# Performance work log

Measured on AMD Instinct MI355X. Metric: run time of the kernel, lower is better.

The kernel has to match this reference:

```python
import jax, jax.numpy as jnp
import numpy as np

B, W, N, K = 8, 16, 40, 10
DN = DL = 128
DE = 128
H = 4
NEG_SLOPE = 0.2


def _build_graph():
    # per-graph ring adjacency: i -> (i+d) % N for d=1..K, in dense_to_sparse order (src-major, dst ascending)
    src0, dst0 = [], []
    for i in range(N):
        ds = sorted(((i + d) % N) for d in range(1, K + 1))
        src0 += [i] * K
        dst0 += ds
    src0 = np.asarray(src0)
    dst0 = np.asarray(dst0)
    G = B * W
    Epg = N * K
    offs = np.arange(G)[:, None] * N
    node_adj = np.stack([(src0[None] + offs).reshape(-1), (dst0[None] + offs).reshape(-1)])
    # line graph: for each node, pair every incoming edge with every outgoing edge (torch repeat/tile order)
    a0, a1, fe = [], [], []
    for num in range(N):
        inc = np.nonzero(dst0 == num)[0]
        out = np.nonzero(src0 == num)[0]
        a0.append(np.repeat(inc, out.size))
        a1.append(np.tile(out, inc.size))
        fe.append(np.full(inc.size * out.size, num))
    a0, a1, fe = np.concatenate(a0), np.concatenate(a1), np.concatenate(fe)
    keep = a0 != a1  # remove_self_loops (no-op here, kept for fidelity)
    a0, a1, fe = a0[keep], a1[keep], fe[keep]
    eoffs = np.arange(G)[:, None] * Epg
    edge_adj = np.stack([(a0[None] + eoffs).reshape(-1), (a1[None] + eoffs).reshape(-1)])
    edge_efea = (fe[None] + offs).reshape(-1)
    return node_adj, edge_adj, edge_efea


def setup_inputs() -> dict:
    key = jax.random.key(0)
    node_adj, edge_adj, edge_efea = _build_graph()
    Epg = N * K
    D1 = DN + DL
    ks = jax.random.split(key, 16)

    def lin(k, fi, fo):
        return jax.random.normal(k, (fi, fo), jnp.float32) / np.sqrt(fi).astype(np.float32)

    return dict(
        x_node=jax.random.normal(ks[0], (B, W, N, DN), jnp.float32),
        x_trace=jax.random.normal(ks[1], (B, W, Epg, DE), jnp.float32),
        x_log=jax.random.normal(ks[2], (B, W, N, DL), jnp.float32),
        node_adj=jnp.asarray(node_adj, jnp.int32),
        edge_adj=jnp.asarray(edge_adj, jnp.int32),
        edge_efea=jnp.asarray(edge_efea, jnp.int32),
        Wl1=lin(ks[3], D1, D1), bl1=jnp.zeros((D1,), jnp.float32),
        Wr1=lin(ks[4], D1, D1), br1=jnp.zeros((D1,), jnp.float32),
        We1=lin(ks[5], DE, D1), be1=jnp.zeros((D1,), jnp.float32),
        att1=jax.random.normal(ks[6], (H, D1 // H), jnp.float32) / np.sqrt(D1 // H).astype(np.float32),
        bias1=jnp.zeros((D1,), jnp.float32),
        Wl2=lin(ks[7], DE, DE), bl2=jnp.zeros((DE,), jnp.float32),
        Wr2=lin(ks[8], DE, DE), br2=jnp.zeros((DE,), jnp.float32),
        We2=lin(ks[9], D1, DE), be2=jnp.zeros((DE,), jnp.float32),
        att2=jax.random.normal(ks[10], (H, DE // H), jnp.float32) / np.sqrt(DE // H).astype(np.float32),
        bias2=jnp.zeros((DE,), jnp.float32),
    )


def _gatv2(x, edge_index, edge_attr, Wl, bl, Wr, br, We, be, att, bias, heads):
    """PyG GATv2Conv (eval mode, add_self_loops=False, concat heads)."""
    n = x.shape[0]
    HC = Wl.shape[1]
    C = HC // heads
    xl = (x @ Wl + bl).reshape(n, heads, C)  # source transform
    xr = (x @ Wr + br).reshape(n, heads, C)  # target transform
    src, dst = edge_index[0], edge_index[1]
    ea = (edge_attr @ We + be).reshape(-1, heads, C)
    m = jax.nn.leaky_relu(xl[src] + xr[dst] + ea, NEG_SLOPE)  # [E,H,C]
    logits = jnp.einsum('ehc,hc->eh', m, att)
    # segment softmax over incoming edges per target node
    mx = jax.ops.segment_max(logits, dst, num_segments=n)
    mx = jnp.where(jnp.isfinite(mx), mx, 0.0)
    ex = jnp.exp(logits - mx[dst])
    den = jax.ops.segment_sum(ex, dst, num_segments=n)
    alpha = ex / (den[dst] + 1e-16)
    out = jax.ops.segment_sum(alpha[:, :, None] * xl[src], dst, num_segments=n)  # [n,H,C]
    return out.reshape(n, HC) + bias


def reference(x_node, x_trace, x_log, node_adj, edge_adj, edge_efea,
              Wl1, bl1, Wr1, br1, We1, be1, att1, bias1,
              Wl2, bl2, Wr2, br2, We2, be2, att2, bias2):
    b, w, n, dn = x_node.shape
    dl = x_log.shape[-1]
    node = jnp.concatenate([x_node, x_log], axis=-1).reshape(-1, dn + dl)  # [G*N, Dn+Dl]
    trace = x_trace.reshape(-1, x_trace.shape[-1])                          # [G*Epg, De]
    node = _gatv2(node, node_adj, trace, Wl1, bl1, Wr1, br1, We1, be1, att1, bias1, H)
    trace = _gatv2(trace, edge_adj, node[edge_efea], Wl2, bl2, Wr2, br2, We2, be2, att2, bias2, H)
    x_node_o = node[:, :dn].reshape(b, w, n, dn)
    x_trace_o = trace.reshape(b, w, -1, trace.shape[-1])
    x_log_o = node[:, dn:].reshape(b, w, n, dl)
    return (x_node_o, x_trace_o, x_log_o)
```

## Files before the change

### kernel.cpp

```cpp
#include <hip/hip_runtime.h>
#include <hip/hip_bf16.h>

#define D1 256
#define DE 128
#define KDEG 10
#define NPG 40
#define EPG 400
#define LOG2E 1.44269504088896340736f

typedef __attribute__((ext_vector_type(8))) short short8;
typedef __attribute__((ext_vector_type(4))) float f32x4;

static inline int cdiv(size_t a, int b) { return (int)((a + b - 1) / b); }
static inline size_t al256(size_t x) { return (x + 255) & ~(size_t)255; }

__device__ __forceinline__ short f2b(float x) {
  __hip_bfloat16 h = __float2bfloat16(x);
  return *reinterpret_cast<short*>(&h);
}

__device__ __forceinline__ short8 cvt8(const float* __restrict__ src) {
  float4 v0 = *(const float4*)src;
  float4 v1 = *(const float4*)(src + 4);
  short8 t;
  t[0] = f2b(v0.x); t[1] = f2b(v0.y); t[2] = f2b(v0.z); t[3] = f2b(v0.w);
  t[4] = f2b(v1.x); t[5] = f2b(v1.y); t[6] = f2b(v1.z); t[7] = f2b(v1.w);
  return t;
}

__global__ __launch_bounds__(256) void k_setup(const float* __restrict__ xn,
                                               const float* __restrict__ xlg,
                                               const float* __restrict__ xtr,
                                               const float* __restrict__ Wl1,
                                               const float* __restrict__ Wr1,
                                               const float* __restrict__ We1,
                                               const float* __restrict__ Wl2,
                                               const float* __restrict__ Wr2,
                                               const float* __restrict__ We2,
                                               const float* __restrict__ bl1,
                                               const float* __restrict__ br1,
                                               const float* __restrict__ be1,
                                               const float* __restrict__ bl2,
                                               const float* __restrict__ br2,
                                               const int* __restrict__ adj,
                                               int* __restrict__ cnt,
                                               int* __restrict__ inc,
                                               short* __restrict__ Xb,
                                               short* __restrict__ xtr_b,
                                               short* __restrict__ WT12,
                                               short* __restrict__ WTall,
                                               short* __restrict__ We2T,
                                               float* __restrict__ blr1,
                                               float* __restrict__ bfull,
                                               int NN, int NE) {
  size_t idx = (size_t)blockIdx.x * 256 + threadIdx.x;
  size_t n;
  n = (size_t)NN * 32;
  if (idx < n) {
    int row = (int)(idx >> 5), q = (int)(idx & 31);
    const float* src = (q < 16) ? &xn[(size_t)row * 128 + q * 8]
                                : &xlg[(size_t)row * 128 + (q - 16) * 8];
    *(short8*)&Xb[(size_t)row * 256 + q * 8] = cvt8(src);
    return;
  }
  idx -= n;
  n = (size_t)NE * 16;
  if (idx < n) {
    *(short8*)&xtr_b[idx * 8] = cvt8(&xtr[idx * 8]);
    return;
  }
  idx -= n;
  n = 512 * 256;
  if (idx < n) {
    int nn = (int)(idx >> 8), k = (int)(idx & 255);
    float v = (nn < 256) ? Wl1[(size_t)k * 256 + nn] : Wr1[(size_t)k * 256 + (nn - 256)];
    WT12[idx] = f2b(v);
    return;
  }
  idx -= n;
  n = 512 * 128;
  if (idx < n) {
    int nn = (int)(idx >> 7), k = (int)(idx & 127);
    float v;
    if (nn < 256)      v = We1[(size_t)k * 256 + nn];
    else if (nn < 384) v = Wl2[(size_t)k * 128 + (nn - 256)];
    else               v = Wr2[(size_t)k * 128 + (nn - 384)];
    WTall[idx] = f2b(v);
    return;
  }
  idx -= n;
  n = 128 * 256;
  if (idx < n) {
    int nn = (int)(idx >> 8), k = (int)(idx & 255);
    We2T[idx] = f2b(We2[(size_t)k * 128 + nn]);
    return;
  }
  idx -= n;
  n = 512;
  if (idx < n) { blr1[idx] = (idx < 256) ? bl1[idx] : br1[idx - 256]; return; }
  idx -= n;
  n = 512;
  if (idx < n) {
    bfull[idx] = (idx < 256) ? be1[idx] : (idx < 384 ? bl2[idx - 256] : br2[idx - 384]);
    return;
  }
  idx -= n;
  n = (size_t)NE;
  if (idx < n) {
    int dst = adj[NE + idx];
    int slot = atomicAdd(&cnt[dst], 1);
    inc[dst * KDEG + slot] = (int)idx;
  }
}

__global__ __launch_bounds__(256) void k_gemm_dual(const short* __restrict__ Xb,
                                                   const short* __restrict__ WT12,
                                                   const float* __restrict__ blr1,
                                                   float* __restrict__ xlr1,
                                                   const short* __restrict__ xtr_b,
                                                   const short* __restrict__ WTl2,
                                                   const float* __restrict__ bia2,
                                                   float* __restrict__ pool2,
                                                   int NN, int NE) {
  __shared__ __align__(16) short As[64][40];
  __shared__ __align__(16) short Bs[64][40];
  const int tid = threadIdx.x;
  const int wave = tid >> 6, lane = tid & 63;
  const int quad = lane >> 4, l16 = lane & 15;
  const short *A, *WT;
  const float* bias;
  float* C;
  int K, N, m0, n0;
  {
    int bid = blockIdx.x;
    if (bid < 8 * (NN / 64)) {
      A = Xb; WT = WT12; bias = blr1; C = xlr1; K = 256; N = 512;
      n0 = (bid & 7) * 64; m0 = (bid >> 3) * 64;
    } else {
      bid -= 8 * (NN / 64);
      A = xtr_b; WT = WTl2; bias = bia2; C = pool2; K = 128; N = 256;
      n0 = (bid & 3) * 64; m0 = (bid >> 2) * 64;
    }
  }
  const int wm = (wave & 1) * 32, wn = (wave >> 1) * 32;
  const int r = tid >> 2, kc = (tid & 3) << 3;
  f32x4 acc[2][2] = {};
  short8 pa = *(const short8*)&A[(size_t)(m0 + r) * K + kc];
  short8 pb = *(const short8*)&WT[(size_t)(n0 + r) * K + kc];
  for (int k0 = 0; k0 < K; k0 += 32) {
    *(short8*)&As[r][kc] = pa;
    *(short8*)&Bs[r][kc] = pb;
    __syncthreads();
    if (k0 + 32 < K) {
      pa = *(const short8*)&A[(size_t)(m0 + r) * K + (k0 + 32 + kc)];
      pb = *(const short8*)&WT[(size_t)(n0 + r) * K + (k0 + 32 + kc)];
    }
    short8 af[2], bf[2];
    #pragma unroll
    for (int mt = 0; mt < 2; ++mt)
      af[mt] = *(const short8*)&As[wm + mt * 16 + l16][quad << 3];
    #pragma unroll
    for (int nt = 0; nt < 2; ++nt)
      bf[nt] = *(const short8*)&Bs[wn + nt * 16 + l16][quad << 3];
    #pragma unroll
    for (int mt = 0; mt < 2; ++mt)
      #pragma unroll
      for (int nt = 0; nt < 2; ++nt)
        acc[mt][nt] = __builtin_amdgcn_mfma_f32_16x16x32_bf16(
            af[mt], bf[nt], acc[mt][nt], 0, 0, 0);
    __syncthreads();
  }
  #pragma unroll
  for (int nt = 0; nt < 2; ++nt) {
    int col = n0 + wn + nt * 16 + l16;
    float bs = bias[col];
    #pragma unroll
    for (int mt = 0; mt < 2; ++mt) {
      int row = m0 + wm + mt * 16 + (quad << 2);
      #pragma unroll
      for (int rr = 0; rr < 4; ++rr)
        C[(size_t)(row + rr) * N + col] = acc[mt][nt][rr] + bs;
    }
  }
}

__global__ __launch_bounds__(256) void k_gemm_mfma64(const short* __restrict__ A,
                                                     const short* __restrict__ WT,
                                                     const float* __restrict__ bias,
                                                     float* __restrict__ C,
                                                     int M, int K, int N) {
  __shared__ __align__(16) short As[64][40];
  __shared__ __align__(16) short Bs[64][40];
  const int tid = threadIdx.x;
  const int wave = tid >> 6, lane = tid & 63;
  const int quad = lane >> 4, l16 = lane & 15;
  const int m0 = blockIdx.y * 64, n0 = blockIdx.x * 64;
  const int wm = (wave & 1) * 32, wn = (wave >> 1) * 32;
  const int r = tid >> 2, kc = (tid & 3) << 3;
  f32x4 acc[2][2] = {};
  short8 pa = *(const short8*)&A[(size_t)(m0 + r) * K + kc];
  short8 pb = *(const short8*)&WT[(size_t)(n0 + r) * K + kc];
  for (int k0 = 0; k0 < K; k0 += 32) {
    *(short8*)&As[r][kc] = pa;
    *(short8*)&Bs[r][kc] = pb;
    __syncthreads();
    if (k0 + 32 < K) {
      pa = *(const short8*)&A[(size_t)(m0 + r) * K + (k0 + 32 + kc)];
      pb = *(const short8*)&WT[(size_t)(n0 + r) * K + (k0 + 32 + kc)];
    }
    short8 af[2], bf[2];
    #pragma unroll
    for (int mt = 0; mt < 2; ++mt)
      af[mt] = *(const short8*)&As[wm + mt * 16 + l16][quad << 3];
    #pragma unroll
    for (int nt = 0; nt < 2; ++nt)
      bf[nt] = *(const short8*)&Bs[wn + nt * 16 + l16][quad << 3];
    #pragma unroll
    for (int mt = 0; mt < 2; ++mt)
      #pragma unroll
      for (int nt = 0; nt < 2; ++nt)
        acc[mt][nt] = __builtin_amdgcn_mfma_f32_16x16x32_bf16(
            af[mt], bf[nt], acc[mt][nt], 0, 0, 0);
    __syncthreads();
  }
  #pragma unroll
  for (int nt = 0; nt < 2; ++nt) {
    int col = n0 + wn + nt * 16 + l16;
    float bs = bias[col];
    #pragma unroll
    for (int mt = 0; mt < 2; ++mt) {
      int row = m0 + wm + mt * 16 + (quad << 2);
      #pragma unroll
      for (int rr = 0; rr < 4; ++rr)
        C[(size_t)(row + rr) * N + col] = acc[mt][nt][rr] + bs;
    }
  }
}

__global__ __launch_bounds__(256) void k_logit(const short* __restrict__ A,
                                               const short* __restrict__ WT,
                                               const float* __restrict__ bfull,
                                               const float* __restrict__ att1,
                                               const int* __restrict__ adj,
                                               const float* __restrict__ xlr1,
                                               float* __restrict__ logit1,
                                               int NE) {
  const int K = 128;
  struct SmemGemm { short As[128][40]; short Bs[128][40]; };
  struct SmemEpi  { int sdst[128]; float sxl[14][132]; float sxr[NPG][132]; };
  __shared__ __align__(16) union { SmemGemm g; SmemEpi e; } sm;
  const int tid = threadIdx.x;
  const int wave = tid >> 6, lane = tid & 63;
  const int quad = lane >> 4, l16 = lane & 15;
  int bid = blockIdx.x;
  int l = (bid & 7) * ((int)gridDim.x >> 3) + (bid >> 3);
  const int n0 = (l & 1) << 7;
  const int m0 = (l >> 1) << 7;
  const int wm = (wave & 1) * 64, wn = (wave >> 1) * 64;
  const int rr0 = tid >> 2, rr1 = (tid + 256) >> 2;
  const int kc = (tid & 3) << 3;
  f32x4 acc[4][4] = {};
  short8 pa0 = *(const short8*)&A[(size_t)(m0 + rr0) * K + kc];
  short8 pb0 = *(const short8*)&WT[(size_t)(n0 + rr0) * K + kc];
  short8 pa1 = *(const short8*)&A[(size_t)(m0 + rr1) * K + kc];
  short8 pb1 = *(const short8*)&WT[(size_t)(n0 + rr1) * K + kc];
  for (int k0 = 0; k0 < K; k0 += 32) {
    *(short8*)&sm.g.As[rr0][kc] = pa0;
    *(short8*)&sm.g.Bs[rr0][kc] = pb0;
    *(short8*)&sm.g.As[rr1][kc] = pa1;
    *(short8*)&sm.g.Bs[rr1][kc] = pb1;
    __syncthreads();
    if (k0 + 32 < K) {
      pa0 = *(const short8*)&A[(size_t)(m0 + rr0) * K + (k0 + 32 + kc)];
      pb0 = *(const short8*)&WT[(size_t)(n0 + rr0) * K + (k0 + 32 + kc)];
      pa1 = *(const short8*)&A[(size_t)(m0 + rr1) * K + (k0 + 32 + kc)];
      pb1 = *(const short8*)&WT[(size_t)(n0 + rr1) * K + (k0 + 32 + kc)];
    }
    short8 af[4], bf[4];
    #pragma unroll
    for (int mt = 0; mt < 4; ++mt)
      af[mt] = *(const short8*)&sm.g.As[wm + mt * 16 + l16][quad << 3];
    #pragma unroll
    for (int nt = 0; nt < 4; ++nt)
      bf[nt] = *(const short8*)&sm.g.Bs[wn + nt * 16 + l16][quad << 3];
    #pragma unroll
    for (int mt = 0; mt < 4; ++mt)
      #pragma unroll
      for (int nt = 0; nt < 4; ++nt)
        acc[mt][nt] = __builtin_amdgcn_mfma_f32_16x16x32_bf16(
            af[mt], bf[nt], acc[mt][nt], 0, 0, 0);
    __syncthreads();
  }
  const int gl = m0 / EPG;
  const int gh = (m0 + 127) / EPG;
  const int slo = m0 / KDEG;
  const int nrl = (m0 + 127) / KDEG - slo + 1;
  if (tid < 128) sm.e.sdst[tid] = adj[NE + m0 + tid];
  for (int s = tid; s < nrl * 128; s += 256) {
    int row = s >> 7, c = s & 127;
    sm.e.sxl[row][c] = xlr1[(size_t)(slo + row) * 512 + n0 + c];
  }
  const int h = (n0 + wn) >> 6;
  float attv[4], bev[4];
  int ccl[4];
  #pragma unroll
  for (int nt = 0; nt < 4; ++nt) {
    int col = n0 + wn + nt * 16 + l16;
    ccl[nt] = col - n0;
    attv[nt] = att1[col] * LOG2E;
    bev[nt] = bfull[col];
  }
  for (int g = gl; g <= gh; ++g) {
    __syncthreads();
    for (int s = tid; s < NPG * 128; s += 256) {
      int row = s >> 7, c = s & 127;
      sm.e.sxr[row][c] = xlr1[(size_t)(g * NPG + row) * 512 + 256 + n0 + c];
    }
    __syncthreads();
    const int elo = g * EPG, ehi = elo + EPG;
    #pragma unroll
    for (int mt = 0; mt < 4; ++mt) {
      #pragma unroll
      for (int r = 0; r < 4; ++r) {
        int le = wm + mt * 16 + (quad << 2) + r;
        int e = m0 + le;
        if (e < elo || e >= ehi) continue;
        int srow = e / KDEG - slo;
        int d = sm.e.sdst[le];
        int drow = d - g * NPG;
        float p = 0.f;
        #pragma unroll
        for (int nt = 0; nt < 4; ++nt) {
          float v = acc[mt][nt][r] + bev[nt] + sm.e.sxl[srow][ccl[nt]]
                  + sm.e.sxr[drow][ccl[nt]];
          v = (v > 0.f) ? v : 0.2f * v;
          p += v * attv[nt];
        }
        p += __shfl_xor(p, 1, 64);
        p += __shfl_xor(p, 2, 64);
        p += __shfl_xor(p, 4, 64);
        p += __shfl_xor(p, 8, 64);
        if (l16 == 0) {
          logit1[(size_t)e * 4 + h] = exp2f(p);
        }
      }
    }
  }
}

__global__ __launch_bounds__(256) void k_agg1(const int* __restrict__ adj,
                                              const int* __restrict__ inc,
                                              const float* __restrict__ xlr1,
                                              const float* __restrict__ logit1,
                                              const float* __restrict__ bias1,
                                              short* __restrict__ nodeoutb,
                                              float* __restrict__ out_node,
                                              float* __restrict__ out_log) {
  int u = blockIdx.x, c = threadIdx.x;
  __shared__ int se[KDEG], ssrc[KDEG];
  __shared__ float slg[KDEG * 4];
  if (c < KDEG) se[c] = inc[u * KDEG + c];
  __syncthreads();
  if (c < KDEG) ssrc[c] = adj[se[c]];
  else if (c >= 64 && c < 64 + KDEG * 4) {
    int t = c - 64;
    slg[t] = logit1[(size_t)se[t >> 2] * 4 + (t & 3)];
  }
  __syncthreads();
  int h = c >> 6;
  float den = 0.f;
  #pragma unroll
  for (int j = 0; j < KDEG; ++j) den += slg[j * 4 + h];
  float rden = 1.f / (den + 1e-16f);
  float acc = 0.f;
  #pragma unroll
  for (int j = 0; j < KDEG; ++j)
    acc += slg[j * 4 + h] * xlr1[(size_t)ssrc[j] * 512 + c];
  float val = acc * rden + bias1[c];
  nodeoutb[(size_t)u * D1 + c] = f2b(val);
  if (c < 128) out_node[(size_t)u * 128 + c] = val;
  else         out_log[(size_t)u * 128 + (c - 128)] = val;
}

__global__ __launch_bounds__(256) void k_gat2_v4(const int* __restrict__ eadj,
                                                 const int* __restrict__ efea,
                                                 const float* __restrict__ pool2,
                                                 const float* __restrict__ nproj,
                                                 const float* __restrict__ att2,
                                                 const float* __restrict__ bias2,
                                                 float* __restrict__ out_trace,
                                                 int NL) {
  int gi = blockIdx.x;
  size_t le0 = (size_t)gi * 100;
  int t = threadIdx.x;
  const int wave = t >> 6, lane = t & 63;
  __shared__ int ein[KDEG], eout[KDEG], nvs;
  __shared__ float xs[KDEG][132];
  __shared__ float rs[KDEG][132];
  __shared__ float as_[DE];
  __shared__ float exs[400];
  __shared__ float rdn[40];
  if (t < KDEG)          ein[t] = eadj[le0 + (size_t)t * KDEG];
  else if (t < 2 * KDEG) eout[t - KDEG] = eadj[(size_t)NL + le0 + (t - KDEG)];
  else if (t == 255)     nvs = efea[le0];
  __syncthreads();
  int nv = nvs;
  for (int s = t; s < 320; s += 256) {
    int j = s >> 5, q = (s & 31) << 2;
    *(float4*)&xs[j][q] = *(const float4*)&pool2[(size_t)ein[j] * 256 + q];
    float4 tr4 = *(const float4*)&pool2[(size_t)eout[j] * 256 + 128 + q];
    float4 ea4 = *(const float4*)&nproj[(size_t)nv * DE + q];
    float4 r;
    r.x = tr4.x + ea4.x; r.y = tr4.y + ea4.y;
    r.z = tr4.z + ea4.z; r.w = tr4.w + ea4.w;
    *(float4*)&rs[j][q] = r;
  }
  if (t < 32) {
    float4 a4 = *(const float4*)&att2[t << 2];
    float4 o;
    o.x = a4.x * LOG2E; o.y = a4.y * LOG2E;
    o.z = a4.z * LOG2E; o.w = a4.w * LOG2E;
    *(float4*)&as_[t << 2] = o;
  }
  __syncthreads();
  {
    int h = wave;
    const float* aa = &as_[h << 5];
    for (int idx = lane; idx < 100; idx += 64) {
      int j = idx / 10;
      int o = idx - j * 10;
      const float* xa = &xs[j][h << 5];
      const float* ra = &rs[o][h << 5];
      float p = 0.f;
      #pragma unroll
      for (int i = 0; i < 32; i += 4) {
        float4 xv = *(const float4*)&xa[i];
        float4 rv = *(const float4*)&ra[i];
        float4 av = *(const float4*)&aa[i];
        float v;
        v = xv.x + rv.x; v = (v > 0.f) ? v : 0.2f * v; p += v * av.x;
        v = xv.y + rv.y; v = (v > 0.f) ? v : 0.2f * v; p += v * av.y;
        v = xv.z + rv.z; v = (v > 0.f) ? v : 0.2f * v; p += v * av.z;
        v = xv.w + rv.w; v = (v > 0.f) ? v : 0.2f * v; p += v * av.w;
      }
      exs[(j * 10 + o) * 4 + h] = exp2f(p);
    }
  }
  __syncthreads();
  if (t < 40) {
    float d = 0.f;
    #pragma unroll
    for (int j = 0; j < KDEG; ++j) d += exs[(j * 10 + (t >> 2)) * 4 + (t & 3)];
    rdn[t] = 1.f / d;
  }
  __syncthreads();
  {
    int c = t & 127, h = c >> 5, oh = (t >> 7) * 5;
    float bsv = bias2[c];
    #pragma unroll
    for (int oo = 0; oo < 5; ++oo) {
      int o = oh + oo;
      float acc = 0.f;
      #pragma unroll
      for (int j = 0; j < KDEG; ++j)
        acc += exs[(j * 10 + o) * 4 + h] * xs[j][c];
      out_trace[(size_t)eout[o] * DE + c] = acc * rdn[o * 4 + h] + bsv;
    }
  }
}

extern "C" void kernel_launch(void* const* d_in, const int* in_sizes, int n_in,
                              void* d_out, int out_size, void* d_ws, size_t ws_size,
                              hipStream_t stream) {
  const float* x_node   = (const float*)d_in[0];
  const float* x_trace  = (const float*)d_in[1];
  const float* x_log    = (const float*)d_in[2];
  const int*   node_adj = (const int*)d_in[3];
  const int*   edge_adj = (const int*)d_in[4];
  const int*   edge_efea= (const int*)d_in[5];
  const float* Wl1 = (const float*)d_in[6];
  const float* bl1 = (const float*)d_in[7];
  const float* Wr1 = (const float*)d_in[8];
  const float* br1 = (const float*)d_in[9];
  const float* We1 = (const float*)d_in[10];
  const float* be1 = (const float*)d_in[11];
  const float* att1 = (const float*)d_in[12];
  const float* bias1 = (const float*)d_in[13];
  const float* Wl2 = (const float*)d_in[14];
  const float* bl2 = (const float*)d_in[15];
  const float* Wr2 = (const float*)d_in[16];
  const float* br2 = (const float*)d_in[17];
  const float* We2 = (const float*)d_in[18];
  const float* be2 = (const float*)d_in[19];
  const float* att2 = (const float*)d_in[20];
  const float* bias2 = (const float*)d_in[21];

  const int NN = in_sizes[0] / 128;
  const int NE = in_sizes[1] / 128;
  const int NL = in_sizes[5];

  char* p = (char*)d_ws;
  float* pool2   = (float*)p; p += al256((size_t)NE * 256 * 4);
  float* xlr1    = (float*)p; p += al256((size_t)NN * 512 * 4);
  short* Xb      = (short*)p; p += al256((size_t)NN * D1 * 2);
  short* xtr_b   = (short*)p; p += al256((size_t)NE * DE * 2);
  short* nodeoutb= (short*)p; p += al256((size_t)NN * D1 * 2);
  float* nproj   = (float*)p; p += al256((size_t)NN * DE * 4);
  float* logit1  = (float*)p; p += al256((size_t)NE * 4 * 4);
  int*   inc     = (int*)p;   p += al256((size_t)NN * KDEG * 4);
  int*   cnt     = (int*)p;   p += al256((size_t)NN * 4);
  short* WT12    = (short*)p; p += al256((size_t)512 * 256 * 2);
  short* WTall   = (short*)p; p += al256((size_t)512 * 128 * 2);
  short* We2T    = (short*)p; p += al256((size_t)128 * 256 * 2);
  float* blr1    = (float*)p; p += al256(512 * 4);
  float* bfull   = (float*)p; p += al256(512 * 4);
  (void)ws_size;

  float* out_node  = (float*)d_out;
  float* out_trace = out_node + (size_t)NN * 128;
  float* out_log   = out_trace + (size_t)NE * 128;

  hipMemsetAsync(cnt, 0, (size_t)NN * 4, stream);
  {
    size_t total = (size_t)NN * 32 + (size_t)NE * 16 +
                   512 * 256 + 512 * 128 + 128 * 256 + 512 + 512 + (size_t)NE;
    k_setup<<<cdiv(total, 256), 256, 0, stream>>>(x_node, x_log, x_trace,
                                                  Wl1, Wr1, We1, Wl2, Wr2, We2,
                                                  bl1, br1, be1, bl2, br2,
                                                  node_adj, cnt, inc,
                                                  Xb, xtr_b,
                                                  WT12, WTall, We2T, blr1, bfull,
                                                  NN, NE);
  }

  k_gemm_dual<<<8 * (NN / 64) + 4 * (NE / 64), 256, 0, stream>>>(
      Xb, WT12, blr1, xlr1,
      xtr_b, WTall + (size_t)256 * 128, bfull + 256, pool2, NN, NE);

  k_logit<<<2 * (NE / 128), 256, 0, stream>>>(xtr_b, WTall, bfull, att1,
                                              node_adj, xlr1, logit1, NE);

  k_agg1<<<NN, 256, 0, stream>>>(node_adj, inc, xlr1, logit1, bias1,
                                 nodeoutb, out_node, out_log);

  k_gemm_mfma64<<<dim3(DE / 64, NN / 64), 256, 0, stream>>>(nodeoutb, We2T, be2,
                                                            nproj, NN, D1, DE);

  k_gat2_v4<<<NN, 256, 0, stream>>>(edge_adj, edge_efea, pool2, nproj,
                                    att2, bias2, out_trace, NL);
}
```

Before: 222.2 us.

## Fuse node aggregation, We2 projection and edge GAT into one kernel

Merges the layer-1 node aggregation, the node-to-edge-feature projection GEMM and the layer-2 GAT into a single per-node kernel. Each block recomputes its node's output and projects it through We2 with scalar fp32 FMAs in shared memory, so the bf16 intermediate, the nproj buffer, the We2 transpose and two kernel launches all go away. The cost is that every block reads the whole fp32 We2 (128 KB) and does a 256x128 matvec on CUDA cores rather than MFMA. That raises per-block latency and L2 traffic, and the projection now runs in fp32 instead of bf16.

```diff
diff --git a/kernel.cpp b/kernel.cpp
--- a/kernel.cpp
+++ b/kernel.cpp
@@ -36,7 +36,6 @@
                                                const float* __restrict__ We1,
                                                const float* __restrict__ Wl2,
                                                const float* __restrict__ Wr2,
-                                               const float* __restrict__ We2,
                                                const float* __restrict__ bl1,
                                                const float* __restrict__ br1,
                                                const float* __restrict__ be1,
@@ -49,7 +48,6 @@
                                                short* __restrict__ xtr_b,
                                                short* __restrict__ WT12,
                                                short* __restrict__ WTall,
-                                               short* __restrict__ We2T,
                                                float* __restrict__ blr1,
                                                float* __restrict__ bfull,
                                                int NN, int NE) {
@@ -86,13 +84,6 @@
     else if (nn < 384) v = Wl2[(size_t)k * 128 + (nn - 256)];
     else               v = Wr2[(size_t)k * 128 + (nn - 384)];
     WTall[idx] = f2b(v);
-    return;
-  }
-  idx -= n;
-  n = 128 * 256;
-  if (idx < n) {
-    int nn = (int)(idx >> 8), k = (int)(idx & 255);
-    We2T[idx] = f2b(We2[(size_t)k * 128 + nn]);
     return;
   }
   idx -= n;
@@ -142,59 +133,6 @@
       n0 = (bid & 3) * 64; m0 = (bid >> 2) * 64;
     }
   }
-  const int wm = (wave & 1) * 32, wn = (wave >> 1) * 32;
-  const int r = tid >> 2, kc = (tid & 3) << 3;
-  f32x4 acc[2][2] = {};
-  short8 pa = *(const short8*)&A[(size_t)(m0 + r) * K + kc];
-  short8 pb = *(const short8*)&WT[(size_t)(n0 + r) * K + kc];
-  for (int k0 = 0; k0 < K; k0 += 32) {
-    *(short8*)&As[r][kc] = pa;
-    *(short8*)&Bs[r][kc] = pb;
-    __syncthreads();
-    if (k0 + 32 < K) {
-      pa = *(const short8*)&A[(size_t)(m0 + r) * K + (k0 + 32 + kc)];
-      pb = *(const short8*)&WT[(size_t)(n0 + r) * K + (k0 + 32 + kc)];
-    }
-    short8 af[2], bf[2];
-    #pragma unroll
-    for (int mt = 0; mt < 2; ++mt)
-      af[mt] = *(const short8*)&As[wm + mt * 16 + l16][quad << 3];
-    #pragma unroll
-    for (int nt = 0; nt < 2; ++nt)
-      bf[nt] = *(const short8*)&Bs[wn + nt * 16 + l16][quad << 3];
-    #pragma unroll
-    for (int mt = 0; mt < 2; ++mt)
-      #pragma unroll
-      for (int nt = 0; nt < 2; ++nt)
-        acc[mt][nt] = __builtin_amdgcn_mfma_f32_16x16x32_bf16(
-            af[mt], bf[nt], acc[mt][nt], 0, 0, 0);
-    __syncthreads();
-  }
-  #pragma unroll
-  for (int nt = 0; nt < 2; ++nt) {
-    int col = n0 + wn + nt * 16 + l16;
-    float bs = bias[col];
-    #pragma unroll
-    for (int mt = 0; mt < 2; ++mt) {
-      int row = m0 + wm + mt * 16 + (quad << 2);
-      #pragma unroll
-      for (int rr = 0; rr < 4; ++rr)
-        C[(size_t)(row + rr) * N + col] = acc[mt][nt][rr] + bs;
-    }
-  }
-}
-
-__global__ __launch_bounds__(256) void k_gemm_mfma64(const short* __restrict__ A,
-                                                     const short* __restrict__ WT,
-                                                     const float* __restrict__ bias,
-                                                     float* __restrict__ C,
-                                                     int M, int K, int N) {
-  __shared__ __align__(16) short As[64][40];
-  __shared__ __align__(16) short Bs[64][40];
-  const int tid = threadIdx.x;
-  const int wave = tid >> 6, lane = tid & 63;
-  const int quad = lane >> 4, l16 = lane & 15;
-  const int m0 = blockIdx.y * 64, n0 = blockIdx.x * 64;
   const int wm = (wave & 1) * 32, wn = (wave >> 1) * 32;
   const int r = tid >> 2, kc = (tid & 3) << 3;
   f32x4 acc[2][2] = {};
@@ -348,53 +286,32 @@
   }
 }
 
-__global__ __launch_bounds__(256) void k_agg1(const int* __restrict__ adj,
-                                              const int* __restrict__ inc,
-                                              const float* __restrict__ xlr1,
-                                              const float* __restrict__ logit1,
-                                              const float* __restrict__ bias1,
-                                              short* __restrict__ nodeoutb,
-                                              float* __restrict__ out_node,
-                                              float* __restrict__ out_log) {
-  int u = blockIdx.x, c = threadIdx.x;
-  __shared__ int se[KDEG], ssrc[KDEG];
-  __shared__ float slg[KDEG * 4];
-  if (c < KDEG) se[c] = inc[u * KDEG + c];
-  __syncthreads();
-  if (c < KDEG) ssrc[c] = adj[se[c]];
-  else if (c >= 64 && c < 64 + KDEG * 4) {
-    int t = c - 64;
-    slg[t] = logit1[(size_t)se[t >> 2] * 4 + (t & 3)];
-  }
-  __syncthreads();
-  int h = c >> 6;
-  float den = 0.f;
-  #pragma unroll
-  for (int j = 0; j < KDEG; ++j) den += slg[j * 4 + h];
-  float rden = 1.f / (den + 1e-16f);
-  float acc = 0.f;
-  #pragma unroll
-  for (int j = 0; j < KDEG; ++j)
-    acc += slg[j * 4 + h] * xlr1[(size_t)ssrc[j] * 512 + c];
-  float val = acc * rden + bias1[c];
-  nodeoutb[(size_t)u * D1 + c] = f2b(val);
-  if (c < 128) out_node[(size_t)u * 128 + c] = val;
-  else         out_log[(size_t)u * 128 + (c - 128)] = val;
-}
-
-__global__ __launch_bounds__(256) void k_gat2_v4(const int* __restrict__ eadj,
-                                                 const int* __restrict__ efea,
-                                                 const float* __restrict__ pool2,
-                                                 const float* __restrict__ nproj,
-                                                 const float* __restrict__ att2,
-                                                 const float* __restrict__ bias2,
-                                                 float* __restrict__ out_trace,
-                                                 int NL) {
+__global__ __launch_bounds__(256) void k_fused2(const int* __restrict__ adj,
+                                                const int* __restrict__ inc,
+                                                const int* __restrict__ eadj,
+                                                const int* __restrict__ efea,
+                                                const float* __restrict__ xlr1,
+                                                const float* __restrict__ logit1,
+                                                const float* __restrict__ bias1,
+                                                const float* __restrict__ pool2,
+                                                const float* __restrict__ We2,
+                                                const float* __restrict__ be2,
+                                                const float* __restrict__ att2,
+                                                const float* __restrict__ bias2,
+                                                float* __restrict__ out_node,
+                                                float* __restrict__ out_log,
+                                                float* __restrict__ out_trace,
+                                                int NL) {
   int gi = blockIdx.x;
   size_t le0 = (size_t)gi * 100;
   int t = threadIdx.x;
   const int wave = t >> 6, lane = t & 63;
   __shared__ int ein[KDEG], eout[KDEG], nvs;
+  __shared__ int se[KDEG], ssrc[KDEG];
+  __shared__ float slg[KDEG * 4];
+  __shared__ float snode[D1];
+  __shared__ float psum[2][DE];
+  __shared__ float np[DE];
   __shared__ float xs[KDEG][132];
   __shared__ float rs[KDEG][132];
   __shared__ float as_[DE];
@@ -404,23 +321,59 @@
   else if (t < 2 * KDEG) eout[t - KDEG] = eadj[(size_t)NL + le0 + (t - KDEG)];
   else if (t == 255)     nvs = efea[le0];
   __syncthreads();
-  int nv = nvs;
+  const int u = nvs;
+  if (t < KDEG) se[t] = inc[u * KDEG + t];
   for (int s = t; s < 320; s += 256) {
     int j = s >> 5, q = (s & 31) << 2;
     *(float4*)&xs[j][q] = *(const float4*)&pool2[(size_t)ein[j] * 256 + q];
-    float4 tr4 = *(const float4*)&pool2[(size_t)eout[j] * 256 + 128 + q];
-    float4 ea4 = *(const float4*)&nproj[(size_t)nv * DE + q];
-    float4 r;
-    r.x = tr4.x + ea4.x; r.y = tr4.y + ea4.y;
-    r.z = tr4.z + ea4.z; r.w = tr4.w + ea4.w;
-    *(float4*)&rs[j][q] = r;
-  }
-  if (t < 32) {
-    float4 a4 = *(const float4*)&att2[t << 2];
+    *(float4*)&rs[j][q] = *(const float4*)&pool2[(size_t)eout[j] * 256 + 128 + q];
+  }
+  if (t >= 192 && t < 224) {
+    int q = t - 192;
+    float4 a4 = *(const float4*)&att2[q << 2];
     float4 o;
     o.x = a4.x * LOG2E; o.y = a4.y * LOG2E;
     o.z = a4.z * LOG2E; o.w = a4.w * LOG2E;
-    *(float4*)&as_[t << 2] = o;
+    *(float4*)&as_[q << 2] = o;
+  }
+  __syncthreads();
+  if (t < KDEG) ssrc[t] = adj[se[t]];
+  else if (t >= 64 && t < 64 + KDEG * 4) {
+    int q = t - 64;
+    slg[q] = logit1[(size_t)se[q >> 2] * 4 + (q & 3)];
+  }
+  __syncthreads();
+  {
+    int h = t >> 6;
+    float den = 0.f;
+    #pragma unroll
+    for (int j = 0; j < KDEG; ++j) den += slg[j * 4 + h];
+    float rden = 1.f / (den + 1e-16f);
+    float acc = 0.f;
+    #pragma unroll
+    for (int j = 0; j < KDEG; ++j)
+      acc += slg[j * 4 + h] * xlr1[(size_t)ssrc[j] * 512 + t];
+    float val = acc * rden + bias1[t];
+    snode[t] = val;
+    if (t < 128) out_node[(size_t)u * 128 + t] = val;
+    else         out_log[(size_t)u * 128 + (t - 128)] = val;
+  }
+  __syncthreads();
+  {
+    int c2 = t & 127, kh = t >> 7;
+    const float* wb = &We2[(size_t)kh * 128 * 128 + c2];
+    float pacc = 0.f;
+    #pragma unroll 4
+    for (int k = 0; k < 128; ++k)
+      pacc += snode[kh * 128 + k] * wb[(size_t)k * 128];
+    psum[kh][c2] = pacc;
+  }
+  __syncthreads();
+  if (t < 128) np[t] = psum[0][t] + psum[1][t] + be2[t];
+  __syncthreads();
+  for (int s = t; s < KDEG * 128; s += 256) {
+    int j = s >> 7, c = s & 127;
+    rs[j][c] += np[c];
   }
   __syncthreads();
   {
@@ -504,14 +457,11 @@
   float* xlr1    = (float*)p; p += al256((size_t)NN * 512 * 4);
   short* Xb      = (short*)p; p += al256((size_t)NN * D1 * 2);
   short* xtr_b   = (short*)p; p += al256((size_t)NE * DE * 2);
-  short* nodeoutb= (short*)p; p += al256((size_t)NN * D1 * 2);
-  float* nproj   = (float*)p; p += al256((size_t)NN * DE * 4);
   float* logit1  = (float*)p; p += al256((size_t)NE * 4 * 4);
   int*   inc     = (int*)p;   p += al256((size_t)NN * KDEG * 4);
   int*   cnt     = (int*)p;   p += al256((size_t)NN * 4);
   short* WT12    = (short*)p; p += al256((size_t)512 * 256 * 2);
   short* WTall   = (short*)p; p += al256((size_t)512 * 128 * 2);
-  short* We2T    = (short*)p; p += al256((size_t)128 * 256 * 2);
   float* blr1    = (float*)p; p += al256(512 * 4);
   float* bfull   = (float*)p; p += al256(512 * 4);
   (void)ws_size;
@@ -523,13 +473,13 @@
   hipMemsetAsync(cnt, 0, (size_t)NN * 4, stream);
   {
     size_t total = (size_t)NN * 32 + (size_t)NE * 16 +
-                   512 * 256 + 512 * 128 + 128 * 256 + 512 + 512 + (size_t)NE;
+                   512 * 256 + 512 * 128 + 512 + 512 + (size_t)NE;
     k_setup<<<cdiv(total, 256), 256, 0, stream>>>(x_node, x_log, x_trace,
-                                                  Wl1, Wr1, We1, Wl2, Wr2, We2,
+                                                  Wl1, Wr1, We1, Wl2, Wr2,
                                                   bl1, br1, be1, bl2, br2,
                                                   node_adj, cnt, inc,
                                                   Xb, xtr_b,
-                                                  WT12, WTall, We2T, blr1, bfull,
+                                                  WT12, WTall, blr1, bfull,
                                                   NN, NE);
   }
 
@@ -540,12 +490,8 @@
   k_logit<<<2 * (NE / 128), 256, 0, stream>>>(xtr_b, WTall, bfull, att1,
                                               node_adj, xlr1, logit1, NE);
 
-  k_agg1<<<NN, 256, 0, stream>>>(node_adj, inc, xlr1, logit1, bias1,
-                                 nodeoutb, out_node, out_log);
-
-  k_gemm_mfma64<<<dim3(DE / 64, NN / 64), 256, 0, stream>>>(nodeoutb, We2T, be2,
-                                                            nproj, NN, D1, DE);
-
-  k_gat2_v4<<<NN, 256, 0, stream>>>(edge_adj, edge_efea, pool2, nproj,
-                                    att2, bias2, out_trace, NL);
-}
+  k_fused2<<<NN, 256, 0, stream>>>(node_adj, inc, edge_adj, edge_efea,
+                                   xlr1, logit1, bias1, pool2, We2, be2,
+                                   att2, bias2, out_node, out_log, out_trace,
+                                   NL);
+}
```

Result: slower. 252.4 us (+13.6%).
